# Kernel tuning notes

Hardware: AMD Instinct MI355X
Metric: run time of the kernel (lower is better)

Reference implementation:

```python
import jax, jax.numpy as jnp
import numpy as np

B, S, DM, H = 4, 2048, 512, 8
DEPTH = DM // H  # 64


def setup_inputs() -> dict:
    key = jax.random.key(0)
    ks = jax.random.split(key, 12)
    sd = 1.0 / np.sqrt(DM)
    return {
        "Q": jax.random.normal(ks[0], (B, S, DM), jnp.float32),
        "K": jax.random.normal(ks[1], (B, S, DM), jnp.float32),
        "V": jax.random.normal(ks[2], (B, S, DM), jnp.float32),
        "mask": jnp.zeros((B, 1, S), jnp.float32),
        "Wq": jax.random.normal(ks[3], (DM, DM), jnp.float32) * sd,
        "bq": jnp.zeros((DM,), jnp.float32),
        "Wk": jax.random.normal(ks[4], (DM, DM), jnp.float32) * sd,
        "bk": jnp.zeros((DM,), jnp.float32),
        "Wv": jax.random.normal(ks[5], (DM, DM), jnp.float32) * sd,
        "bv": jnp.zeros((DM,), jnp.float32),
        "Wo": jax.random.normal(ks[6], (DM, DM), jnp.float32) * sd,
        "bo": jnp.zeros((DM,), jnp.float32),
    }


def reference(Q, K, V, mask, Wq, bq, Wk, bk, Wv, bv, Wo, bo):
    # Linear projections to [B, S, DM]
    q = Q @ Wq + bq
    k = K @ Wk + bk
    v = V @ Wv + bv
    # Contiguous channel slices of size depth == reshape to [B, S, H, depth]
    q = q.reshape(B, S, H, DEPTH).transpose(0, 2, 1, 3)  # [B,H,S,d]
    k = k.reshape(B, S, H, DEPTH).transpose(0, 2, 1, 3)
    v = v.reshape(B, S, H, DEPTH).transpose(0, 2, 1, 3)
    scale = 1.0 / jnp.sqrt(jnp.asarray(DEPTH, q.dtype))
    scores = jnp.einsum("bhqd,bhkd->bhqk", q, k) * scale  # [B,H,S,S]
    # mask [B,1,S] broadcasts over heads and query positions
    scores = scores + mask[:, None, :, :] * -1e9
    att_ws = jax.nn.softmax(scores, axis=-1)  # [B,H,S,S]
    ctx = jnp.einsum("bhqk,bhkd->bhqd", att_ws, v)  # [B,H,S,d]
    ctx = ctx.transpose(0, 2, 1, 3).reshape(B, S, DM)  # concat heads
    Y = ctx @ Wo + bo
    return Y, att_ws
```

## Files before the change

kernel.cpp:

```cpp
#include <hip/hip_runtime.h>


typedef __bf16 bf16;
typedef __bf16 bf16x8 __attribute__((ext_vector_type(8)));
typedef float f32x4 __attribute__((ext_vector_type(4)));

constexpr int BATCH = 4;
constexpr int SEQ = 2048;
constexpr int DMODEL = 512;
constexpr int NHEAD = 8;
constexpr int HDIM = 64;
constexpr int MTOT = BATCH * SEQ;
constexpr long YELEMS = (long)MTOT * DMODEL;
constexpr long WELEMS = (long)DMODEL * DMODEL;
constexpr float LOG2E = 1.44269504f;

__device__ __forceinline__ f32x4 mfma_bf16(bf16x8 a, bf16x8 b, f32x4 c) {
  return __builtin_amdgcn_mfma_f32_16x16x32_bf16(a, b, c, 0, 0, 0);
}

__global__ void detect_k(const unsigned int* q, int* flag) {
  unsigned u = q[threadIdx.x];
  int e = (u >> 7) & 0xff;
  unsigned long long m = __ballot(e >= 0x60 && e <= 0x9f);
  if (threadIdx.x == 0) flag[0] = (__popcll(m) >= 48) ? 1 : 0;
}

__global__ __launch_bounds__(256) void cvt_qkv_k(
    const void* __restrict__ q, const void* __restrict__ k,
    const void* __restrict__ v, bf16* __restrict__ qb, bf16* __restrict__ kb,
    bf16* __restrict__ vb, const int* flag) {
  const int z = blockIdx.y;
  const void* src = (z == 0) ? q : (z == 1) ? k : v;
  bf16* dst = (z == 0) ? qb : (z == 1) ? kb : vb;
  const long i8 = ((long)blockIdx.x * 256 + threadIdx.x) * 8;
  if (*flag) {
    *(uint4*)(dst + i8) = *(const uint4*)((const bf16*)src + i8);
  } else {
    const float* s = (const float*)src + i8;
    const float4 a = *(const float4*)s;
    const float4 b = *(const float4*)(s + 4);
    bf16x8 o;
    o[0] = (bf16)a.x; o[1] = (bf16)a.y; o[2] = (bf16)a.z; o[3] = (bf16)a.w;
    o[4] = (bf16)b.x; o[5] = (bf16)b.y; o[6] = (bf16)b.z; o[7] = (bf16)b.w;
    *(bf16x8*)(dst + i8) = o;
  }
}

__global__ void cvt_mb_k(const void* __restrict__ mask,
                         const void* __restrict__ b0,
                         const void* __restrict__ b1,
                         const void* __restrict__ b2,
                         const void* __restrict__ b3,
                         float* __restrict__ maskf, bf16* __restrict__ bias_c,
                         const int* flag) {
  const int f = *flag;
  const int i = blockIdx.x * 256 + threadIdx.x;
  if (i < BATCH * SEQ) {
    const float m = f ? (float)((const bf16*)mask)[i] : ((const float*)mask)[i];
    maskf[i] = m * (-1e9f * LOG2E);
  } else {
    const int j = i - BATCH * SEQ;
    const int w = j >> 9;
    const void* s = (w == 0) ? b0 : (w == 1) ? b1 : (w == 2) ? b2 : b3;
    const int o = j & 511;
    bias_c[j] = f ? ((const bf16*)s)[o] : (bf16)((const float*)s)[o];
  }
}

__global__ __launch_bounds__(256) void transpose_w4_k(
    const void* __restrict__ wq, const void* __restrict__ wk,
    const void* __restrict__ wv, const void* __restrict__ wo,
    bf16* __restrict__ wqt, bf16* __restrict__ wkt, bf16* __restrict__ wvt,
    bf16* __restrict__ wot, const int* flag) {
  __shared__ bf16 t[32][33];
  const int z = blockIdx.z;
  const void* w = (z == 0) ? wq : (z == 1) ? wk : (z == 2) ? wv : wo;
  bf16* wt = (z == 0) ? wqt : (z == 1) ? wkt : (z == 2) ? wvt : wot;
  const int f = *flag;
  const int bx = blockIdx.x * 32, by = blockIdx.y * 32;
  const int tx = threadIdx.x & 31, ty = threadIdx.x >> 5;
  for (int i = ty; i < 32; i += 8) {
    const long idx = (long)(by + i) * DMODEL + bx + tx;
    t[i][tx] = f ? ((const bf16*)w)[idx] : (bf16)((const float*)w)[idx];
  }
  __syncthreads();
  for (int i = ty; i < 32; i += 8)
    wt[(long)(bx + i) * DMODEL + by + tx] = t[tx][i];
}

__global__ __launch_bounds__(256) void proj_gemm(
    const bf16* __restrict__ X, const bf16* __restrict__ Wt,
    const bf16* __restrict__ bias, void* __restrict__ out, int mode,
    const int* flag) {
  __shared__ __attribute__((aligned(16))) bf16 As[64][72];
  __shared__ __attribute__((aligned(16))) bf16 Bs[64][72];
  const int f = *flag;
  const int r0 = blockIdx.x * 64;
  const int c0 = blockIdx.y * 64;
  const int tid = threadIdx.x;
  const int wave = tid >> 6, lane = tid & 63;
  const int quad = lane >> 4, l16 = lane & 15;
  const int srow = tid >> 3, scb = (tid & 7) * 8;

  f32x4 acc[4] = {};
  for (int k0 = 0; k0 < DMODEL; k0 += 64) {
    __syncthreads();
    *(uint4*)&As[srow][scb] =
        *(const uint4*)(X + (long)(r0 + srow) * DMODEL + k0 + scb);
    *(uint4*)&As[srow + 32][scb] =
        *(const uint4*)(X + (long)(r0 + srow + 32) * DMODEL + k0 + scb);
    *(uint4*)&Bs[srow][scb] =
        *(const uint4*)(Wt + (long)(c0 + srow) * DMODEL + k0 + scb);
    *(uint4*)&Bs[srow + 32][scb] =
        *(const uint4*)(Wt + (long)(c0 + srow + 32) * DMODEL + k0 + scb);
    __syncthreads();
    const int m = wave * 16 + l16;
#pragma unroll
    for (int kk = 0; kk < 64; kk += 32) {
      bf16x8 a = *(const bf16x8*)&As[m][kk + quad * 8];
#pragma unroll
      for (int n = 0; n < 4; n++) {
        bf16x8 bb8 = *(const bf16x8*)&Bs[n * 16 + l16][kk + quad * 8];
        acc[n] = mfma_bf16(a, bb8, acc[n]);
      }
    }
  }

  __syncthreads();
  const bool f32out = (mode == 0) && !f;
#pragma unroll
  for (int n = 0; n < 4; n++) {
    const float bvv = (float)bias[c0 + n * 16 + l16];
#pragma unroll
    for (int r = 0; r < 4; r++) {
      const float v = acc[n][r] + bvv;
      const int ml = wave * 16 + quad * 4 + r;
      const int nl = n * 16 + l16;
      if (f32out) {
        ((float*)out)[(long)(r0 + ml) * DMODEL + c0 + nl] = v;
      } else if (mode == 2) {
        As[nl][ml] = (bf16)v;
      } else {
        As[ml][nl] = (bf16)v;
      }
    }
  }
  if (f32out) return;
  __syncthreads();

  const int rb = r0 >> 11;
  const int s0 = r0 & (SEQ - 1);
  const int hh = c0 >> 6;
  bf16* ob = (bf16*)out;
#pragma unroll
  for (int i = 0; i < 2; i++) {
    const int mrow = srow + i * 32;
    long idx;
    if (mode == 0) {
      idx = (long)(r0 + mrow) * DMODEL + c0 + scb;
    } else if (mode == 1) {
      idx = (((long)(rb * NHEAD + hh) * SEQ) + s0 + mrow) * HDIM + scb;
    } else {
      idx = (((long)(rb * NHEAD + hh) * HDIM) + mrow) * SEQ + s0 + scb;
    }
    *(uint4*)(ob + idx) = *(const uint4*)&As[mrow][scb];
  }
}

__global__ __launch_bounds__(256) void attn_k(
    const bf16* __restrict__ qh, const bf16* __restrict__ kh,
    const bf16* __restrict__ vt, const float* __restrict__ maskf,
    bf16* __restrict__ attB, float* __restrict__ attF, bf16* __restrict__ ctx,
    const int* flag) {
  __shared__ __attribute__((aligned(16))) bf16 qs[64][72];
  __shared__ __attribute__((aligned(16))) bf16 ks[64][72];
  __shared__ __attribute__((aligned(16))) bf16 vs[64][72];
  __shared__ __attribute__((aligned(16))) bf16 ps[64][72];

  const int f = *flag;
  const int bh = blockIdx.y;
  const int bb = bh >> 3, hh = bh & 7;
  const int q0 = blockIdx.x * 64;
  const int tid = threadIdx.x;
  const int wave = tid >> 6, lane = tid & 63;
  const int quad = lane >> 4, l16 = lane & 15;
  const int srow = tid >> 3, scb = (tid & 7) * 8;
  const float scale2 = 0.125f * LOG2E;

  const bf16* qp = qh + ((long)bh * SEQ + q0) * HDIM;
  const bf16* kp = kh + (long)bh * SEQ * HDIM;
  const bf16* vp = vt + (long)bh * HDIM * SEQ;
  const float* mp = maskf + (long)bb * SEQ;

  *(uint4*)&qs[srow][scb] = *(const uint4*)(qp + (long)srow * HDIM + scb);
  *(uint4*)&qs[srow + 32][scb] =
      *(const uint4*)(qp + (long)(srow + 32) * HDIM + scb);

  float m_ln[4], l_ln[4];
#pragma unroll
  for (int r = 0; r < 4; r++) { m_ln[r] = -3e38f; l_ln[r] = 0.f; }
  const int mrow = wave * 16 + l16;

  for (int t = 0; t < SEQ / 64; t++) {
    __syncthreads();
    const bf16* kt = kp + (long)t * 64 * HDIM;
    *(uint4*)&ks[srow][scb] = *(const uint4*)(kt + (long)srow * HDIM + scb);
    *(uint4*)&ks[srow + 32][scb] =
        *(const uint4*)(kt + (long)(srow + 32) * HDIM + scb);
    float mv[4];
#pragma unroll
    for (int n = 0; n < 4; n++) mv[n] = mp[t * 64 + n * 16 + l16];
    __syncthreads();
    f32x4 sc[4] = {};
#pragma unroll
    for (int kk = 0; kk < 64; kk += 32) {
      bf16x8 a = *(const bf16x8*)&qs[mrow][kk + quad * 8];
#pragma unroll
      for (int n = 0; n < 4; n++) {
        bf16x8 bb8 = *(const bf16x8*)&ks[n * 16 + l16][kk + quad * 8];
        sc[n] = mfma_bf16(a, bb8, sc[n]);
      }
    }
#pragma unroll
    for (int r = 0; r < 4; r++) {
      const float v0 = fmaf(sc[0][r], scale2, mv[0]);
      const float v1 = fmaf(sc[1][r], scale2, mv[1]);
      const float v2 = fmaf(sc[2][r], scale2, mv[2]);
      const float v3 = fmaf(sc[3][r], scale2, mv[3]);
      const float mx = fmaxf(fmaxf(v0, v1), fmaxf(v2, v3));
      const float mnew = fmaxf(m_ln[r], mx);
      l_ln[r] = l_ln[r] * exp2f(m_ln[r] - mnew) + exp2f(v0 - mnew) +
                exp2f(v1 - mnew) + exp2f(v2 - mnew) + exp2f(v3 - mnew);
      m_ln[r] = mnew;
    }
  }

  float m_i[4], rcl[4];
#pragma unroll
  for (int r = 0; r < 4; r++) {
    float mr = m_ln[r];
#pragma unroll
    for (int o = 1; o < 16; o <<= 1) mr = fmaxf(mr, __shfl_xor(mr, o, 64));
    float lr = l_ln[r] * exp2f(m_ln[r] - mr);
#pragma unroll
    for (int o = 1; o < 16; o <<= 1) lr += __shfl_xor(lr, o, 64);
    m_i[r] = mr;
    rcl[r] = 1.f / lr;
  }

  f32x4 oacc[4] = {};
  const long abase = ((long)bh * SEQ + q0) * SEQ;

  for (int t = 0; t < SEQ / 64; t++) {
    __syncthreads();
    const bf16* kt = kp + (long)t * 64 * HDIM;
    *(uint4*)&ks[srow][scb] = *(const uint4*)(kt + (long)srow * HDIM + scb);
    *(uint4*)&ks[srow + 32][scb] =
        *(const uint4*)(kt + (long)(srow + 32) * HDIM + scb);
    *(uint4*)&vs[srow][scb] =
        *(const uint4*)(vp + (long)srow * SEQ + t * 64 + scb);
    *(uint4*)&vs[srow + 32][scb] =
        *(const uint4*)(vp + (long)(srow + 32) * SEQ + t * 64 + scb);
    float mv[4];
#pragma unroll
    for (int n = 0; n < 4; n++) mv[n] = mp[t * 64 + n * 16 + l16];
    __syncthreads();
    f32x4 sc[4] = {};
#pragma unroll
    for (int kk = 0; kk < 64; kk += 32) {
      bf16x8 a = *(const bf16x8*)&qs[mrow][kk + quad * 8];
#pragma unroll
      for (int n = 0; n < 4; n++) {
        bf16x8 bb8 = *(const bf16x8*)&ks[n * 16 + l16][kk + quad * 8];
        sc[n] = mfma_bf16(a, bb8, sc[n]);
      }
    }
#pragma unroll
    for (int r = 0; r < 4; r++) {
      const int prow = wave * 16 + quad * 4 + r;
#pragma unroll
      for (int n = 0; n < 4; n++) {
        const float p =
            exp2f(fmaf(sc[n][r], scale2, mv[n]) - m_i[r]) * rcl[r];
        ps[prow][n * 16 + l16] = (bf16)p;
        if (!f) attF[abase + (long)prow * SEQ + t * 64 + n * 16 + l16] = p;
      }
    }
    __syncthreads();
#pragma unroll
    for (int kk = 0; kk < 64; kk += 32) {
      bf16x8 a = *(const bf16x8*)&ps[wave * 16 + l16][kk + quad * 8];
#pragma unroll
      for (int n = 0; n < 4; n++) {
        bf16x8 bb8 = *(const bf16x8*)&vs[n * 16 + l16][kk + quad * 8];
        oacc[n] = mfma_bf16(a, bb8, oacc[n]);
      }
    }
    if (f) {
#pragma unroll
      for (int i = 0; i < 2; i++) {
        const int ci = lane + i * 64;
        const int rr = ci >> 3, cc = (ci & 7) * 8;
        *(uint4*)(attB + abase + (long)(wave * 16 + rr) * SEQ + t * 64 + cc) =
            *(const uint4*)&ps[wave * 16 + rr][cc];
      }
    }
  }

#pragma unroll
  for (int n = 0; n < 4; n++) {
#pragma unroll
    for (int r = 0; r < 4; r++) {
      const int s = q0 + wave * 16 + quad * 4 + r;
      const int d = n * 16 + l16;
      ctx[((long)bb * SEQ + s) * DMODEL + hh * HDIM + d] = (bf16)oacc[n][r];
    }
  }
}

extern "C" void kernel_launch(void* const* d_in, const int* in_sizes, int n_in,
                              void* d_out, int out_size, void* d_ws,
                              size_t ws_size, hipStream_t stream) {
  const void* Q = d_in[0];
  const void* K = d_in[1];
  const void* V = d_in[2];
  const void* mask = d_in[3];
  const void* Wq = d_in[4];
  const void* bq = d_in[5];
  const void* Wk = d_in[6];
  const void* bk = d_in[7];
  const void* Wv = d_in[8];
  const void* bv = d_in[9];
  const void* Wo = d_in[10];
  const void* bo = d_in[11];

  char* ob = (char*)d_out;
  bf16* attB = (bf16*)(ob + 2 * YELEMS);
  float* attF = (float*)(ob + 4 * YELEMS);
  bf16* qh = (bf16*)ob;

  bf16* stg = (bf16*)(ob + 4 * YELEMS);
  bf16* wqt = stg;
  bf16* wkt = wqt + WELEMS;
  bf16* wvt = wkt + WELEMS;
  bf16* qb = wvt + WELEMS;
  bf16* kb = qb + YELEMS;
  bf16* vb = kb + YELEMS;

  char* wb = (char*)d_ws;
  int* flag = (int*)wb;
  float* maskf = (float*)(wb + 16);
  bf16* bias_c = (bf16*)(wb + 16 + 32768);
  bf16* bq_c = bias_c;
  bf16* bk_c = bq_c + 512;
  bf16* bv_c = bk_c + 512;
  bf16* bo_c = bv_c + 512;
  bf16* kh = (bf16*)(wb + 16 + 32768 + 4096);
  bf16* vtb = kh + YELEMS;
  bf16* ctx = vtb + YELEMS;
  bf16* wot = ctx + YELEMS;

  dim3 tb(256);
  detect_k<<<1, 64, 0, stream>>>((const unsigned int*)Q, flag);

  cvt_mb_k<<<40, tb, 0, stream>>>(mask, bq, bk, bv, bo, maskf, bias_c, flag);
  cvt_qkv_k<<<dim3(YELEMS / (256 * 8), 3), tb, 0, stream>>>(Q, K, V, qb, kb,
                                                            vb, flag);
  transpose_w4_k<<<dim3(DMODEL / 32, DMODEL / 32, 4), tb, 0, stream>>>(
      Wq, Wk, Wv, Wo, wqt, wkt, wvt, wot, flag);

  dim3 gp(MTOT / 64, DMODEL / 64);
  proj_gemm<<<gp, tb, 0, stream>>>(qb, wqt, bq_c, qh, 1, flag);
  proj_gemm<<<gp, tb, 0, stream>>>(kb, wkt, bk_c, kh, 1, flag);
  proj_gemm<<<gp, tb, 0, stream>>>(vb, wvt, bv_c, vtb, 2, flag);

  attn_k<<<dim3(SEQ / 64, BATCH * NHEAD), tb, 0, stream>>>(
      qh, kh, vtb, maskf, attB, attF, ctx, flag);

  proj_gemm<<<gp, tb, 0, stream>>>(ctx, wot, bo_c, d_out, 0, flag);
}
```

Baseline: 795.7 us.

## Widen attention blocks to 128 queries with register-prefetched K/V tiles

Each attention block now covers 128 query rows with 8 waves, so every K/V tile loaded into shared memory serves twice as many queries. Q fragments stay in registers instead of shared memory, the mask row is staged once in shared memory, and the next K/V tile is prefetched into registers while the current one is computed. The barrier between writing P and the PV MFMA is dropped, since each wave only reads back its own rows of ps. The cost is more registers per thread and half as many blocks in the grid.

New measurement: 765.8 us. 1.04x faster.

```diff
diff --git a/kernel.cpp b/kernel.cpp
--- a/kernel.cpp
+++ b/kernel.cpp
@@ -168,59 +168,64 @@
   }
 }
 
-__global__ __launch_bounds__(256) void attn_k(
+__global__ __launch_bounds__(512) void attn_k(
     const bf16* __restrict__ qh, const bf16* __restrict__ kh,
     const bf16* __restrict__ vt, const float* __restrict__ maskf,
     bf16* __restrict__ attB, float* __restrict__ attF, bf16* __restrict__ ctx,
     const int* flag) {
-  __shared__ __attribute__((aligned(16))) bf16 qs[64][72];
   __shared__ __attribute__((aligned(16))) bf16 ks[64][72];
   __shared__ __attribute__((aligned(16))) bf16 vs[64][72];
-  __shared__ __attribute__((aligned(16))) bf16 ps[64][72];
+  __shared__ __attribute__((aligned(16))) bf16 ps[128][72];
+  __shared__ float msk[SEQ];
 
   const int f = *flag;
   const int bh = blockIdx.y;
   const int bb = bh >> 3, hh = bh & 7;
-  const int q0 = blockIdx.x * 64;
+  const int q0 = blockIdx.x * 128;
   const int tid = threadIdx.x;
   const int wave = tid >> 6, lane = tid & 63;
   const int quad = lane >> 4, l16 = lane & 15;
-  const int srow = tid >> 3, scb = (tid & 7) * 8;
+  const int srow = tid >> 3;
+  const int scb = (tid & 7) * 8;
   const float scale2 = 0.125f * LOG2E;
+  constexpr int NT = SEQ / 64;
 
   const bf16* qp = qh + ((long)bh * SEQ + q0) * HDIM;
   const bf16* kp = kh + (long)bh * SEQ * HDIM;
   const bf16* vp = vt + (long)bh * HDIM * SEQ;
   const float* mp = maskf + (long)bb * SEQ;
 
-  *(uint4*)&qs[srow][scb] = *(const uint4*)(qp + (long)srow * HDIM + scb);
-  *(uint4*)&qs[srow + 32][scb] =
-      *(const uint4*)(qp + (long)(srow + 32) * HDIM + scb);
+  ((float4*)msk)[tid] = ((const float4*)mp)[tid];
+
+  const int rq = wave * 16 + l16;
+  const bf16x8 qa0 = *(const bf16x8*)(qp + (long)rq * HDIM + quad * 8);
+  const bf16x8 qa1 = *(const bf16x8*)(qp + (long)rq * HDIM + 32 + quad * 8);
+
+  uint4 kreg = *(const uint4*)(kp + (long)srow * HDIM + scb);
 
   float m_ln[4], l_ln[4];
 #pragma unroll
   for (int r = 0; r < 4; r++) { m_ln[r] = -3e38f; l_ln[r] = 0.f; }
-  const int mrow = wave * 16 + l16;
-
-  for (int t = 0; t < SEQ / 64; t++) {
-    __syncthreads();
-    const bf16* kt = kp + (long)t * 64 * HDIM;
-    *(uint4*)&ks[srow][scb] = *(const uint4*)(kt + (long)srow * HDIM + scb);
-    *(uint4*)&ks[srow + 32][scb] =
-        *(const uint4*)(kt + (long)(srow + 32) * HDIM + scb);
+
+  for (int t = 0; t < NT; t++) {
+    __syncthreads();
+    *(uint4*)&ks[srow][scb] = kreg;
+    if (t + 1 < NT)
+      kreg = *(const uint4*)(kp + ((long)(t + 1) * 64 + srow) * HDIM + scb);
+    __syncthreads();
     float mv[4];
 #pragma unroll
-    for (int n = 0; n < 4; n++) mv[n] = mp[t * 64 + n * 16 + l16];
-    __syncthreads();
+    for (int n = 0; n < 4; n++) mv[n] = msk[t * 64 + n * 16 + l16];
     f32x4 sc[4] = {};
 #pragma unroll
-    for (int kk = 0; kk < 64; kk += 32) {
-      bf16x8 a = *(const bf16x8*)&qs[mrow][kk + quad * 8];
-#pragma unroll
-      for (int n = 0; n < 4; n++) {
-        bf16x8 bb8 = *(const bf16x8*)&ks[n * 16 + l16][kk + quad * 8];
-        sc[n] = mfma_bf16(a, bb8, sc[n]);
-      }
+    for (int n = 0; n < 4; n++) {
+      bf16x8 b0 = *(const bf16x8*)&ks[n * 16 + l16][quad * 8];
+      sc[n] = mfma_bf16(qa0, b0, sc[n]);
+    }
+#pragma unroll
+    for (int n = 0; n < 4; n++) {
+      bf16x8 b1 = *(const bf16x8*)&ks[n * 16 + l16][32 + quad * 8];
+      sc[n] = mfma_bf16(qa1, b1, sc[n]);
     }
 #pragma unroll
     for (int r = 0; r < 4; r++) {
@@ -236,6 +241,9 @@
     }
   }
 
+  kreg = *(const uint4*)(kp + (long)srow * HDIM + scb);
+  uint4 vreg = *(const uint4*)(vp + (long)srow * SEQ + scb);
+
   float m_i[4], rcl[4];
 #pragma unroll
   for (int r = 0; r < 4; r++) {
@@ -252,29 +260,28 @@
   f32x4 oacc[4] = {};
   const long abase = ((long)bh * SEQ + q0) * SEQ;
 
-  for (int t = 0; t < SEQ / 64; t++) {
-    __syncthreads();
-    const bf16* kt = kp + (long)t * 64 * HDIM;
-    *(uint4*)&ks[srow][scb] = *(const uint4*)(kt + (long)srow * HDIM + scb);
-    *(uint4*)&ks[srow + 32][scb] =
-        *(const uint4*)(kt + (long)(srow + 32) * HDIM + scb);
-    *(uint4*)&vs[srow][scb] =
-        *(const uint4*)(vp + (long)srow * SEQ + t * 64 + scb);
-    *(uint4*)&vs[srow + 32][scb] =
-        *(const uint4*)(vp + (long)(srow + 32) * SEQ + t * 64 + scb);
+  for (int t = 0; t < NT; t++) {
+    __syncthreads();
+    *(uint4*)&ks[srow][scb] = kreg;
+    *(uint4*)&vs[srow][scb] = vreg;
+    if (t + 1 < NT) {
+      kreg = *(const uint4*)(kp + ((long)(t + 1) * 64 + srow) * HDIM + scb);
+      vreg = *(const uint4*)(vp + (long)srow * SEQ + (t + 1) * 64 + scb);
+    }
+    __syncthreads();
     float mv[4];
 #pragma unroll
-    for (int n = 0; n < 4; n++) mv[n] = mp[t * 64 + n * 16 + l16];
-    __syncthreads();
+    for (int n = 0; n < 4; n++) mv[n] = msk[t * 64 + n * 16 + l16];
     f32x4 sc[4] = {};
 #pragma unroll
-    for (int kk = 0; kk < 64; kk += 32) {
-      bf16x8 a = *(const bf16x8*)&qs[mrow][kk + quad * 8];
-#pragma unroll
-      for (int n = 0; n < 4; n++) {
-        bf16x8 bb8 = *(const bf16x8*)&ks[n * 16 + l16][kk + quad * 8];
-        sc[n] = mfma_bf16(a, bb8, sc[n]);
-      }
+    for (int n = 0; n < 4; n++) {
+      bf16x8 b0 = *(const bf16x8*)&ks[n * 16 + l16][quad * 8];
+      sc[n] = mfma_bf16(qa0, b0, sc[n]);
+    }
+#pragma unroll
+    for (int n = 0; n < 4; n++) {
+      bf16x8 b1 = *(const bf16x8*)&ks[n * 16 + l16][32 + quad * 8];
+      sc[n] = mfma_bf16(qa1, b1, sc[n]);
     }
 #pragma unroll
     for (int r = 0; r < 4; r++) {
@@ -287,7 +294,6 @@
         if (!f) attF[abase + (long)prow * SEQ + t * 64 + n * 16 + l16] = p;
       }
     }
-    __syncthreads();
 #pragma unroll
     for (int kk = 0; kk < 64; kk += 32) {
       bf16x8 a = *(const bf16x8*)&ps[wave * 16 + l16][kk + quad * 8];
@@ -375,7 +381,7 @@
   proj_gemm<<<gp, tb, 0, stream>>>(kb, wkt, bk_c, kh, 1, flag);
   proj_gemm<<<gp, tb, 0, stream>>>(vb, wvt, bv_c, vtb, 2, flag);
 
-  attn_k<<<dim3(SEQ / 64, BATCH * NHEAD), tb, 0, stream>>>(
+  attn_k<<<dim3(SEQ / 128, BATCH * NHEAD), dim3(512), 0, stream>>>(
       qh, kh, vtb, maskf, attB, attF, ctx, flag);
 
   proj_gemm<<<gp, tb, 0, stream>>>(ctx, wot, bo_c, d_out, 0, flag);
```
